# Kernel optimization log

Hardware: AMD Instinct MI355X
Metric: run time of the kernel (lower is better)

The kernel has to match this reference:

```python
import jax, jax.numpy as jnp
import numpy as np

B, D, C = 2048, 512, 50000
MARGIN = 0.3
SCALE = 30.0
EPS = 1e-12


def setup_inputs() -> dict:
    key = jax.random.key(0)
    k1, k2, k3 = jax.random.split(key, 3)
    embeddings = jax.random.normal(k1, (B, D), dtype=jnp.float32)
    labels = jax.random.randint(k2, (B,), 0, C, dtype=jnp.int64)
    # Xavier-uniform init for weight (num_classes, in_features)
    limit = float(np.sqrt(6.0 / (C + D)))
    weight = jax.random.uniform(k3, (C, D), dtype=jnp.float32, minval=-limit, maxval=limit)
    return {"embeddings": embeddings, "labels": labels, "weight": weight}


def _l2_normalize(x, axis):
    # Matches torch F.normalize(p=2, eps=1e-12): x / max(||x||, eps)
    norm = jnp.sqrt(jnp.sum(x * x, axis=axis, keepdims=True))
    return x / jnp.maximum(norm, EPS)


def reference(embeddings, labels, weight):
    emb_n = _l2_normalize(embeddings, axis=1)            # (B, D)
    w_n = _l2_normalize(weight, axis=1)                  # (C, D)
    cos = jnp.einsum("bd,cd->bc", emb_n, w_n)            # (B, C)
    # margin subtract at label index (avoid dense one-hot materialization)
    rows = jnp.arange(cos.shape[0])
    phi = cos.at[rows, labels].add(-MARGIN)
    logits = phi * SCALE
    # cross-entropy with mean reduction
    logp = jax.nn.log_softmax(logits, axis=-1)
    nll = -jnp.take_along_axis(logp, labels[:, None], axis=-1)[:, 0]
    return jnp.mean(nll)
```

## Files before the change

### kernel.cpp

```cpp
#include <hip/hip_runtime.h>
#include <hip/hip_bf16.h>
#include <math.h>
#include <stdint.h>


#define B_ROWS    2048
#define D_DIM     512
#define C_CLASSES 50000
#define C_PAD     50176
#define NCHUNK    112
#define CH_COLS   448
#define NSTRIP    14
#define ARC_MARGIN 0.3f
#define ARC_SCALE  30.0f
#define ARC_EPS    1e-12f
#define K_LOG2E_S  43.2808512f

#define OFF_WQ    0u
#define OFF_EMBQ  25690112u
#define OFF_WINV  26738688u
#define OFF_EINV  26938688u
#define OFF_PART  26946880u
#define OFF_FINP  27864384u

typedef __attribute__((ext_vector_type(8))) int   i32x8;
typedef __attribute__((ext_vector_type(4))) int   i32x4;
typedef __attribute__((ext_vector_type(4))) float f32x4;

typedef __attribute__((address_space(1))) const unsigned int g_u32;
typedef __attribute__((address_space(3))) unsigned int       l_u32;

__device__ __forceinline__ void gload_lds16(const void* g, void* l) {
    g_u32* gp = (g_u32*)(uintptr_t)g;
    l_u32* lp = (l_u32*)(uintptr_t)l;
    __builtin_amdgcn_global_load_lds(gp, lp, 16, 0, 0);
}

__global__ __launch_bounds__(256) void k_prep(const float* __restrict__ emb,
                                              const float* __restrict__ weight,
                                              uint8_t* __restrict__ embq,
                                              uint8_t* __restrict__ wq,
                                              float* __restrict__ einv,
                                              float* __restrict__ winv,
                                              float* __restrict__ out) {
    int wave = blockIdx.x * (blockDim.x >> 6) + (threadIdx.x >> 6);
    int lane = threadIdx.x & 63;
    int g0   = wave << 3;

    const float* src;
    uint8_t* dst;
    float* invout;
    if (g0 >= C_PAD) {
        int row = g0 - C_PAD;
        src = emb + (size_t)row * D_DIM;
        dst = embq + (size_t)row * D_DIM;
        invout = einv + row;
    } else if (g0 >= C_CLASSES) {
        int2 z = make_int2(0, 0);
        #pragma unroll
        for (int r = 0; r < 8; ++r)
            *(int2*)(wq + (size_t)(g0 + r) * D_DIM + lane * 8) = z;
        return;
    } else {
        src = weight + (size_t)g0 * D_DIM;
        dst = wq + (size_t)g0 * D_DIM;
        invout = winv + g0;
    }

    const float4* r4 = (const float4*)src;
    float4 v[16];
    #pragma unroll
    for (int r = 0; r < 8; ++r) {
        v[2 * r]     = r4[r * 128 + lane * 2];
        v[2 * r + 1] = r4[r * 128 + lane * 2 + 1];
    }

    #pragma unroll
    for (int r = 0; r < 8; ++r) {
        float4 v0 = v[2 * r], v1 = v[2 * r + 1];
        float s = v0.x*v0.x + v0.y*v0.y + v0.z*v0.z + v0.w*v0.w
                + v1.x*v1.x + v1.y*v1.y + v1.z*v1.z + v1.w*v1.w;
        #pragma unroll
        for (int off = 32; off; off >>= 1) s += __shfl_xor(s, off);
        float rn = 1.0f / fmaxf(sqrtf(s), ARC_EPS);
        if (lane == 0) invout[r] = rn;
        int p0 = __builtin_amdgcn_cvt_pk_fp8_f32(v0.x * rn, v0.y * rn, 0, false);
        p0     = __builtin_amdgcn_cvt_pk_fp8_f32(v0.z * rn, v0.w * rn, p0, true);
        int p1 = __builtin_amdgcn_cvt_pk_fp8_f32(v1.x * rn, v1.y * rn, 0, false);
        p1     = __builtin_amdgcn_cvt_pk_fp8_f32(v1.z * rn, v1.w * rn, p1, true);
        *(int2*)(dst + (size_t)r * D_DIM + lane * 8) = make_int2(p0, p1);
    }
}

struct TrueT  { static constexpr bool value = true;  };
struct FalseT { static constexpr bool value = false; };

__global__ __launch_bounds__(256) void k_gemm(const uint8_t* __restrict__ embq,
                                              const uint8_t* __restrict__ wq,
                                              float* __restrict__ partials) {
    __shared__ __align__(16) uint8_t Bs[2][16384];

    const int tid  = threadIdx.x;
    const int w    = tid >> 6;
    const int lane = tid & 63;
    const int c    = lane & 15;
    const int q    = lane >> 4;

    const int id  = blockIdx.x;
    const int xcd = id & 7;
    const int s   = id >> 3;
    const int ci  = s % 14;
    const int rb  = s / 14;
    const int chunk = xcd * 14 + ci;
    const int b0 = rb * 128;
    const int n0 = chunk * CH_COLS;

    const int r0 = b0 + w * 32;
    i32x8 afA[4], afB[4];
    #pragma unroll
    for (int kt = 0; kt < 4; ++kt) {
        const uint8_t* pa = embq + (size_t)(r0 + c) * D_DIM + kt * 128 + q * 32;
        const uint8_t* pb = embq + (size_t)(r0 + 16 + c) * D_DIM + kt * 128 + q * 32;
        i32x4 alo = *(const i32x4*)pa;
        i32x4 ahi = *(const i32x4*)(pa + 16);
        i32x4 blo = *(const i32x4*)pb;
        i32x4 bhi = *(const i32x4*)(pb + 16);
        afA[kt] = (i32x8){alo[0], alo[1], alo[2], alo[3], ahi[0], ahi[1], ahi[2], ahi[3]};
        afB[kt] = (i32x8){blo[0], blo[1], blo[2], blo[3], bhi[0], bhi[1], bhi[2], bhi[3]};
    }

    const int srow = c;
    const int skc  = q;
    auto stage = [&](uint8_t* dst, int st) {
        const uint8_t* base = wq + (size_t)(n0 + st * 32) * D_DIM;
        #pragma unroll
        for (int t = 0; t < 4; ++t) {
            const int p  = w * 4 + t;
            const int cb = p >> 3;
            const int h  = p & 7;
            gload_lds16(base + (size_t)(cb * 16 + srow) * D_DIM + (h * 4 + skc) * 16,
                        dst + cb * 8192 + h * 1024);
        }
    };

    f32x4 rs0 = (f32x4){0.f, 0.f, 0.f, 0.f};
    f32x4 rs1 = (f32x4){0.f, 0.f, 0.f, 0.f};

    auto compute = [&](const uint8_t* buf, int st, auto maskTag) {
        constexpr bool MASK = decltype(maskTag)::value;
        #pragma unroll
        for (int cb = 0; cb < 2; ++cb) {
            f32x4 a0 = (f32x4){0.f, 0.f, 0.f, 0.f};
            f32x4 a1 = (f32x4){0.f, 0.f, 0.f, 0.f};
            #pragma unroll
            for (int kt = 0; kt < 4; ++kt) {
                const uint8_t* p = buf + cb * 8192 + (kt * 8 + 2 * q) * 256 + c * 16;
                i32x4 lo = *(const i32x4*)p;
                i32x4 hi = *(const i32x4*)(p + 256);
                i32x8 bf = (i32x8){lo[0], lo[1], lo[2], lo[3],
                                   hi[0], hi[1], hi[2], hi[3]};
                a0 = __builtin_amdgcn_mfma_scale_f32_16x16x128_f8f6f4(
                        afA[kt], bf, a0, 0, 0, 0, 127, 0, 127);
                a1 = __builtin_amdgcn_mfma_scale_f32_16x16x128_f8f6f4(
                        afB[kt], bf, a1, 0, 0, 0, 127, 0, 127);
            }
            bool pad = false;
            if (MASK) pad = (n0 + st * 32 + cb * 16 + c) >= C_CLASSES;
            #pragma unroll
            for (int reg = 0; reg < 4; ++reg) {
                float t0 = __builtin_amdgcn_exp2f(fmaf(a0[reg], K_LOG2E_S, -K_LOG2E_S));
                float t1 = __builtin_amdgcn_exp2f(fmaf(a1[reg], K_LOG2E_S, -K_LOG2E_S));
                if (MASK && pad) { t0 = 0.f; t1 = 0.f; }
                rs0[reg] += t0;
                rs1[reg] += t1;
            }
        }
    };

    auto run = [&](auto maskTag) {
        stage(&Bs[0][0], 0);
        __syncthreads();
        #pragma unroll 1
        for (int st = 0; st < NSTRIP; st += 2) {
            stage(&Bs[1][0], st + 1);
            compute(&Bs[0][0], st, maskTag);
            __syncthreads();
            if (st + 2 < NSTRIP) stage(&Bs[0][0], st + 2);
            compute(&Bs[1][0], st + 1, maskTag);
            __syncthreads();
        }
    };
    if (chunk == NCHUNK - 1) run(TrueT{}); else run(FalseT{});

    #pragma unroll
    for (int off = 1; off < 16; off <<= 1) {
        #pragma unroll
        for (int reg = 0; reg < 4; ++reg) {
            rs0[reg] += __shfl_xor(rs0[reg], off);
            rs1[reg] += __shfl_xor(rs1[reg], off);
        }
    }
    if (c == 0) {
        #pragma unroll
        for (int reg = 0; reg < 4; ++reg) {
            partials[(size_t)(r0 + q * 4 + reg) * NCHUNK + chunk]      = rs0[reg];
            partials[(size_t)(r0 + 16 + q * 4 + reg) * NCHUNK + chunk] = rs1[reg];
        }
    }
}

__global__ __launch_bounds__(256) void k_fin(const float* __restrict__ emb,
                                             const float* __restrict__ weight,
                                             const float* __restrict__ einv,
                                             const float* __restrict__ winv,
                                             const int* __restrict__ labels,
                                             const float* __restrict__ partials,
                                             float* __restrict__ finpart) {
    __shared__ float sm[8];
    int w    = threadIdx.x >> 6;
    int lane = threadIdx.x & 63;
    int b0   = blockIdx.x * 8 + w * 2;

    int lab[2] = {labels[b0], labels[b0 + 1]};
    float4 e0[2], e1[2], w0[2], w1[2];
    float p0[2], p1[2];
    #pragma unroll
    for (int r = 0; r < 2; ++r) {
        const float4* e  = (const float4*)(emb + (size_t)(b0 + r) * D_DIM);
        const float4* wt = (const float4*)(weight + (size_t)lab[r] * D_DIM);
        e0[r] = e[lane];  e1[r] = e[lane + 64];
        w0[r] = wt[lane]; w1[r] = wt[lane + 64];
        p0[r] = partials[(size_t)(b0 + r) * NCHUNK + lane];
        p1[r] = (lane + 64 < NCHUNK)
              ? partials[(size_t)(b0 + r) * NCHUNK + lane + 64] : 0.f;
    }

    #pragma unroll
    for (int r = 0; r < 2; ++r) {
        float dot = e0[r].x*w0[r].x + e0[r].y*w0[r].y + e0[r].z*w0[r].z + e0[r].w*w0[r].w
                  + e1[r].x*w1[r].x + e1[r].y*w1[r].y + e1[r].z*w1[r].z + e1[r].w*w1[r].w;
        float ls = p0[r] + p1[r];
        #pragma unroll
        for (int off = 32; off; off >>= 1) {
            dot += __shfl_xor(dot, off);
            ls  += __shfl_xor(ls, off);
        }
        if (lane == 0) {
            int b = b0 + r;
            float cosv   = dot * einv[b] * winv[lab[r]];
            float l_orig = ARC_SCALE * cosv;
            float l_adj  = ARC_SCALE * (cosv - ARC_MARGIN);
            float s_adj = ls - __expf(l_orig - ARC_SCALE) + __expf(l_adj - ARC_SCALE);
            sm[w * 2 + r] = ARC_SCALE + logf(s_adj) - l_adj;
        }
    }
    __syncthreads();
    if (threadIdx.x == 0) {
        float t = 0.f;
        #pragma unroll
        for (int i = 0; i < 8; ++i) t += sm[i];
        finpart[blockIdx.x] = t;
    }
}

__global__ __launch_bounds__(256) void k_sum(const float* __restrict__ finpart,
                                             float* __restrict__ out) {
    __shared__ float sm[4];
    int w = threadIdx.x >> 6, lane = threadIdx.x & 63;
    float v = finpart[threadIdx.x];
    #pragma unroll
    for (int off = 32; off; off >>= 1) v += __shfl_xor(v, off);
    if (lane == 0) sm[w] = v;
    __syncthreads();
    if (threadIdx.x == 0)
        out[0] = (sm[0] + sm[1] + sm[2] + sm[3]) * (1.0f / (float)B_ROWS);
}

extern "C" void kernel_launch(void* const* d_in, const int* in_sizes, int n_in,
                              void* d_out, int out_size, void* d_ws, size_t ws_size,
                              hipStream_t stream) {
    const float* emb    = (const float*)d_in[0];
    const int*   labels = (const int*)d_in[1];
    const float* weight = (const float*)d_in[2];
    float* out = (float*)d_out;

    char* ws = (char*)d_ws;
    uint8_t* wq    = (uint8_t*)(ws + OFF_WQ);
    uint8_t* embq  = (uint8_t*)(ws + OFF_EMBQ);
    float* winv     = (float*)(ws + OFF_WINV);
    float* einv     = (float*)(ws + OFF_EINV);
    float* partials = (float*)(ws + OFF_PART);
    float* finpart  = (float*)(ws + OFF_FINP);

    k_prep<<<(C_PAD + B_ROWS) / 32, 256, 0, stream>>>(emb, weight, embq, wq,
                                                      einv, winv, out);

    k_gemm<<<1792, 256, 0, stream>>>(embq, wq, partials);

    k_fin<<<B_ROWS / 8, 256, 0, stream>>>(emb, weight, einv, winv, labels,
                                          partials, finpart);
    k_sum<<<1, 256, 0, stream>>>(finpart, out);
}
```

Baseline: 234.2 us.

## Widen GEMM strip to 64 columns with 2x2 wave layout; fuse final sum via ticket

The GEMM block now stages 64 weight columns per strip into a 32KB double buffer. Its four waves are arranged 2 rows x 2 column-halves, each wave holding 64 embedding rows (16 fp8 A fragments) and issuing 4 MFMAs per B fragment load. This doubles A-fragment reuse per LDS read, and the partial sums table doubles to 224 columns. The separate single-block sum kernel is removed: the last finishing block of k_fin, picked with an atomic ticket that k_prep resets, does the final reduction. This saves one launch but raises register pressure and LDS use, which may lower occupancy.

```diff
diff --git a/kernel.cpp b/kernel.cpp
--- a/kernel.cpp
+++ b/kernel.cpp
@@ -10,7 +10,8 @@
 #define C_PAD     50176
 #define NCHUNK    112
 #define CH_COLS   448
-#define NSTRIP    14
+#define NSTRIP    7
+#define NPART     224
 #define ARC_MARGIN 0.3f
 #define ARC_SCALE  30.0f
 #define ARC_EPS    1e-12f
@@ -21,7 +22,8 @@
 #define OFF_WINV  26738688u
 #define OFF_EINV  26938688u
 #define OFF_PART  26946880u
-#define OFF_FINP  27864384u
+#define OFF_FINP  28781888u
+#define OFF_TICK  28782912u
 
 typedef __attribute__((ext_vector_type(8))) int   i32x8;
 typedef __attribute__((ext_vector_type(4))) int   i32x4;
@@ -42,7 +44,8 @@
                                               uint8_t* __restrict__ wq,
                                               float* __restrict__ einv,
                                               float* __restrict__ winv,
-                                              float* __restrict__ out) {
+                                              unsigned int* __restrict__ ticket) {
+    if (blockIdx.x == 0 && threadIdx.x == 0) *ticket = 0u;
     int wave = blockIdx.x * (blockDim.x >> 6) + (threadIdx.x >> 6);
     int lane = threadIdx.x & 63;
     int g0   = wave << 3;
@@ -98,13 +101,15 @@
 __global__ __launch_bounds__(256) void k_gemm(const uint8_t* __restrict__ embq,
                                               const uint8_t* __restrict__ wq,
                                               float* __restrict__ partials) {
-    __shared__ __align__(16) uint8_t Bs[2][16384];
+    __shared__ __align__(16) uint8_t Bs[2][32768];
 
     const int tid  = threadIdx.x;
     const int w    = tid >> 6;
     const int lane = tid & 63;
     const int c    = lane & 15;
     const int q    = lane >> 4;
+    const int rh   = w >> 1;
+    const int ch   = w & 1;
 
     const int id  = blockIdx.x;
     const int xcd = id & 7;
@@ -115,64 +120,75 @@
     const int b0 = rb * 128;
     const int n0 = chunk * CH_COLS;
 
-    const int r0 = b0 + w * 32;
-    i32x8 afA[4], afB[4];
-    #pragma unroll
-    for (int kt = 0; kt < 4; ++kt) {
-        const uint8_t* pa = embq + (size_t)(r0 + c) * D_DIM + kt * 128 + q * 32;
-        const uint8_t* pb = embq + (size_t)(r0 + 16 + c) * D_DIM + kt * 128 + q * 32;
-        i32x4 alo = *(const i32x4*)pa;
-        i32x4 ahi = *(const i32x4*)(pa + 16);
-        i32x4 blo = *(const i32x4*)pb;
-        i32x4 bhi = *(const i32x4*)(pb + 16);
-        afA[kt] = (i32x8){alo[0], alo[1], alo[2], alo[3], ahi[0], ahi[1], ahi[2], ahi[3]};
-        afB[kt] = (i32x8){blo[0], blo[1], blo[2], blo[3], bhi[0], bhi[1], bhi[2], bhi[3]};
-    }
-
-    const int srow = c;
-    const int skc  = q;
+    const int r0 = b0 + rh * 64;
+    i32x8 af[4][4];
+    #pragma unroll
+    for (int rg = 0; rg < 4; ++rg) {
+        const uint8_t* pr = embq + (size_t)(r0 + rg * 16 + c) * D_DIM;
+        #pragma unroll
+        for (int kt = 0; kt < 4; ++kt) {
+            const uint8_t* pa = pr + kt * 128 + q * 32;
+            i32x4 lo = *(const i32x4*)pa;
+            i32x4 hi = *(const i32x4*)(pa + 16);
+            af[rg][kt] = (i32x8){lo[0], lo[1], lo[2], lo[3],
+                                 hi[0], hi[1], hi[2], hi[3]};
+        }
+    }
+
     auto stage = [&](uint8_t* dst, int st) {
-        const uint8_t* base = wq + (size_t)(n0 + st * 32) * D_DIM;
-        #pragma unroll
-        for (int t = 0; t < 4; ++t) {
-            const int p  = w * 4 + t;
-            const int cb = p >> 3;
+        const uint8_t* base = wq + (size_t)(n0 + st * 64) * D_DIM;
+        #pragma unroll
+        for (int t = 0; t < 8; ++t) {
+            const int p  = w * 8 + t;
+            const int cg = p >> 3;
             const int h  = p & 7;
-            gload_lds16(base + (size_t)(cb * 16 + srow) * D_DIM + (h * 4 + skc) * 16,
-                        dst + cb * 8192 + h * 1024);
+            gload_lds16(base + (size_t)(cg * 16 + c) * D_DIM + (h * 4 + q) * 16,
+                        dst + cg * 8192 + h * 1024);
         }
     };
 
-    f32x4 rs0 = (f32x4){0.f, 0.f, 0.f, 0.f};
-    f32x4 rs1 = (f32x4){0.f, 0.f, 0.f, 0.f};
+    f32x4 rs[4];
+    #pragma unroll
+    for (int rg = 0; rg < 4; ++rg) rs[rg] = (f32x4){0.f, 0.f, 0.f, 0.f};
 
     auto compute = [&](const uint8_t* buf, int st, auto maskTag) {
         constexpr bool MASK = decltype(maskTag)::value;
         #pragma unroll
         for (int cb = 0; cb < 2; ++cb) {
+            const int cg = ch * 2 + cb;
             f32x4 a0 = (f32x4){0.f, 0.f, 0.f, 0.f};
             f32x4 a1 = (f32x4){0.f, 0.f, 0.f, 0.f};
+            f32x4 a2 = (f32x4){0.f, 0.f, 0.f, 0.f};
+            f32x4 a3 = (f32x4){0.f, 0.f, 0.f, 0.f};
             #pragma unroll
             for (int kt = 0; kt < 4; ++kt) {
-                const uint8_t* p = buf + cb * 8192 + (kt * 8 + 2 * q) * 256 + c * 16;
+                const uint8_t* p = buf + cg * 8192 + (kt * 8 + 2 * q) * 256 + c * 16;
                 i32x4 lo = *(const i32x4*)p;
                 i32x4 hi = *(const i32x4*)(p + 256);
                 i32x8 bf = (i32x8){lo[0], lo[1], lo[2], lo[3],
                                    hi[0], hi[1], hi[2], hi[3]};
                 a0 = __builtin_amdgcn_mfma_scale_f32_16x16x128_f8f6f4(
-                        afA[kt], bf, a0, 0, 0, 0, 127, 0, 127);
+                        af[0][kt], bf, a0, 0, 0, 0, 127, 0, 127);
                 a1 = __builtin_amdgcn_mfma_scale_f32_16x16x128_f8f6f4(
-                        afB[kt], bf, a1, 0, 0, 0, 127, 0, 127);
+                        af[1][kt], bf, a1, 0, 0, 0, 127, 0, 127);
+                a2 = __builtin_amdgcn_mfma_scale_f32_16x16x128_f8f6f4(
+                        af[2][kt], bf, a2, 0, 0, 0, 127, 0, 127);
+                a3 = __builtin_amdgcn_mfma_scale_f32_16x16x128_f8f6f4(
+                        af[3][kt], bf, a3, 0, 0, 0, 127, 0, 127);
             }
             bool pad = false;
-            if (MASK) pad = (n0 + st * 32 + cb * 16 + c) >= C_CLASSES;
+            if (MASK) pad = (n0 + st * 64 + cg * 16 + c) >= C_CLASSES;
             #pragma unroll
             for (int reg = 0; reg < 4; ++reg) {
                 float t0 = __builtin_amdgcn_exp2f(fmaf(a0[reg], K_LOG2E_S, -K_LOG2E_S));
                 float t1 = __builtin_amdgcn_exp2f(fmaf(a1[reg], K_LOG2E_S, -K_LOG2E_S));
-                if (MASK && pad) { t0 = 0.f; t1 = 0.f; }
-                rs0[reg] += t0;
-                rs1[reg] += t1;
+                float t2 = __builtin_amdgcn_exp2f(fmaf(a2[reg], K_LOG2E_S, -K_LOG2E_S));
+                float t3 = __builtin_amdgcn_exp2f(fmaf(a3[reg], K_LOG2E_S, -K_LOG2E_S));
+                if (MASK && pad) { t0 = 0.f; t1 = 0.f; t2 = 0.f; t3 = 0.f; }
+                rs[0][reg] += t0;
+                rs[1][reg] += t1;
+                rs[2][reg] += t2;
+                rs[3][reg] += t3;
             }
         }
     };
@@ -182,30 +198,34 @@
         __syncthreads();
         #pragma unroll 1
         for (int st = 0; st < NSTRIP; st += 2) {
-            stage(&Bs[1][0], st + 1);
+            if (st + 1 < NSTRIP) stage(&Bs[1][0], st + 1);
             compute(&Bs[0][0], st, maskTag);
             __syncthreads();
             if (st + 2 < NSTRIP) stage(&Bs[0][0], st + 2);
-            compute(&Bs[1][0], st + 1, maskTag);
-            __syncthreads();
+            if (st + 1 < NSTRIP) {
+                compute(&Bs[1][0], st + 1, maskTag);
+                __syncthreads();
+            }
         }
     };
     if (chunk == NCHUNK - 1) run(TrueT{}); else run(FalseT{});
 
     #pragma unroll
-    for (int off = 1; off < 16; off <<= 1) {
-        #pragma unroll
-        for (int reg = 0; reg < 4; ++reg) {
-            rs0[reg] += __shfl_xor(rs0[reg], off);
-            rs1[reg] += __shfl_xor(rs1[reg], off);
-        }
-    }
+    for (int off = 1; off < 16; off <<= 1)
+        #pragma unroll
+        for (int rg = 0; rg < 4; ++rg)
+            #pragma unroll
+            for (int reg = 0; reg < 4; ++reg)
+                rs[rg][reg] += __shfl_xor(rs[rg][reg], off);
+
     if (c == 0) {
-        #pragma unroll
-        for (int reg = 0; reg < 4; ++reg) {
-            partials[(size_t)(r0 + q * 4 + reg) * NCHUNK + chunk]      = rs0[reg];
-            partials[(size_t)(r0 + 16 + q * 4 + reg) * NCHUNK + chunk] = rs1[reg];
-        }
+        const int pcol = chunk * 2 + ch;
+        #pragma unroll
+        for (int rg = 0; rg < 4; ++rg)
+            #pragma unroll
+            for (int reg = 0; reg < 4; ++reg)
+                partials[(size_t)(r0 + rg * 16 + q * 4 + reg) * NPART + pcol]
+                    = rs[rg][reg];
     }
 }
 
@@ -215,31 +235,37 @@
                                              const float* __restrict__ winv,
                                              const int* __restrict__ labels,
                                              const float* __restrict__ partials,
-                                             float* __restrict__ finpart) {
+                                             float* __restrict__ finpart,
+                                             unsigned int* __restrict__ ticket,
+                                             float* __restrict__ out) {
     __shared__ float sm[8];
+    __shared__ int is_last;
     int w    = threadIdx.x >> 6;
     int lane = threadIdx.x & 63;
     int b0   = blockIdx.x * 8 + w * 2;
 
     int lab[2] = {labels[b0], labels[b0 + 1]};
     float4 e0[2], e1[2], w0[2], w1[2];
-    float p0[2], p1[2];
+    float p[2][4];
     #pragma unroll
     for (int r = 0; r < 2; ++r) {
         const float4* e  = (const float4*)(emb + (size_t)(b0 + r) * D_DIM);
         const float4* wt = (const float4*)(weight + (size_t)lab[r] * D_DIM);
         e0[r] = e[lane];  e1[r] = e[lane + 64];
         w0[r] = wt[lane]; w1[r] = wt[lane + 64];
-        p0[r] = partials[(size_t)(b0 + r) * NCHUNK + lane];
-        p1[r] = (lane + 64 < NCHUNK)
-              ? partials[(size_t)(b0 + r) * NCHUNK + lane + 64] : 0.f;
+        #pragma unroll
+        for (int t = 0; t < 4; ++t) {
+            int idx = lane + t * 64;
+            p[r][t] = (idx < NPART)
+                    ? partials[(size_t)(b0 + r) * NPART + idx] : 0.f;
+        }
     }
 
     #pragma unroll
     for (int r = 0; r < 2; ++r) {
         float dot = e0[r].x*w0[r].x + e0[r].y*w0[r].y + e0[r].z*w0[r].z + e0[r].w*w0[r].w
                   + e1[r].x*w1[r].x + e1[r].y*w1[r].y + e1[r].z*w1[r].z + e1[r].w*w1[r].w;
-        float ls = p0[r] + p1[r];
+        float ls = p[r][0] + p[r][1] + p[r][2] + p[r][3];
         #pragma unroll
         for (int off = 32; off; off >>= 1) {
             dot += __shfl_xor(dot, off);
@@ -260,20 +286,22 @@
         #pragma unroll
         for (int i = 0; i < 8; ++i) t += sm[i];
         finpart[blockIdx.x] = t;
-    }
-}
-
-__global__ __launch_bounds__(256) void k_sum(const float* __restrict__ finpart,
-                                             float* __restrict__ out) {
-    __shared__ float sm[4];
-    int w = threadIdx.x >> 6, lane = threadIdx.x & 63;
-    float v = finpart[threadIdx.x];
-    #pragma unroll
-    for (int off = 32; off; off >>= 1) v += __shfl_xor(v, off);
-    if (lane == 0) sm[w] = v;
+        __threadfence();
+        unsigned int old = atomicAdd(ticket, 1u);
+        is_last = (old == gridDim.x - 1) ? 1 : 0;
+    }
     __syncthreads();
-    if (threadIdx.x == 0)
-        out[0] = (sm[0] + sm[1] + sm[2] + sm[3]) * (1.0f / (float)B_ROWS);
+    if (is_last) {
+        __threadfence();
+        volatile const float* fp = finpart;
+        float v = fp[threadIdx.x];
+        #pragma unroll
+        for (int off = 32; off; off >>= 1) v += __shfl_xor(v, off);
+        if (lane == 0) sm[w] = v;
+        __syncthreads();
+        if (threadIdx.x == 0)
+            out[0] = (sm[0] + sm[1] + sm[2] + sm[3]) * (1.0f / (float)B_ROWS);
+    }
 }
 
 extern "C" void kernel_launch(void* const* d_in, const int* in_sizes, int n_in,
@@ -291,13 +319,13 @@
     float* einv     = (float*)(ws + OFF_EINV);
     float* partials = (float*)(ws + OFF_PART);
     float* finpart  = (float*)(ws + OFF_FINP);
+    unsigned int* ticket = (unsigned int*)(ws + OFF_TICK);
 
     k_prep<<<(C_PAD + B_ROWS) / 32, 256, 0, stream>>>(emb, weight, embq, wq,
-                                                      einv, winv, out);
+                                                      einv, winv, ticket);
 
     k_gemm<<<1792, 256, 0, stream>>>(embq, wq, partials);
 
     k_fin<<<B_ROWS / 8, 256, 0, stream>>>(emb, weight, einv, winv, labels,
-                                          partials, finpart);
-    k_sum<<<1, 256, 0, stream>>>(finpart, out);
-}
+                                          partials, finpart, ticket, out);
+}
```

Result: slower. 276.7 us (+18.2%).

## Triple-buffer GEMM LDS staging and fold final sum into fin kernel

Applied to the files above, without the earlier changes.

The GEMM's weight-tile staging moves from a double buffer with two block barriers per strip pair to a three-slot ring. Each strip now uses a single barrier with an explicit vmcnt wait, so loads run two strips ahead of compute. Separately, the single-block k_sum launch is dropped: k_fin blocks take an atomic ticket and the last block performs the final reduction, saving one kernel launch. This raises LDS use to 48KB per block, which may lower occupancy, and relies on a ticket that k_prep resets.

```diff
diff --git a/kernel.cpp b/kernel.cpp
--- a/kernel.cpp
+++ b/kernel.cpp
@@ -22,6 +22,7 @@
 #define OFF_EINV  26938688u
 #define OFF_PART  26946880u
 #define OFF_FINP  27864384u
+#define OFF_TICK  27865408u
 
 typedef __attribute__((ext_vector_type(8))) int   i32x8;
 typedef __attribute__((ext_vector_type(4))) int   i32x4;
@@ -42,7 +43,8 @@
                                               uint8_t* __restrict__ wq,
                                               float* __restrict__ einv,
                                               float* __restrict__ winv,
-                                              float* __restrict__ out) {
+                                              unsigned int* __restrict__ ticket) {
+    if (blockIdx.x == 0 && threadIdx.x == 0) *ticket = 0u;
     int wave = blockIdx.x * (blockDim.x >> 6) + (threadIdx.x >> 6);
     int lane = threadIdx.x & 63;
     int g0   = wave << 3;
@@ -98,7 +100,7 @@
 __global__ __launch_bounds__(256) void k_gemm(const uint8_t* __restrict__ embq,
                                               const uint8_t* __restrict__ wq,
                                               float* __restrict__ partials) {
-    __shared__ __align__(16) uint8_t Bs[2][16384];
+    __shared__ __align__(16) uint8_t Bs[3][16384];
 
     const int tid  = threadIdx.x;
     const int w    = tid >> 6;
@@ -129,16 +131,14 @@
         afB[kt] = (i32x8){blo[0], blo[1], blo[2], blo[3], bhi[0], bhi[1], bhi[2], bhi[3]};
     }
 
-    const int srow = c;
-    const int skc  = q;
     auto stage = [&](uint8_t* dst, int st) {
-        const uint8_t* base = wq + (size_t)(n0 + st * 32) * D_DIM;
+        const uint8_t* base_ = wq + (size_t)(n0 + st * 32) * D_DIM;
         #pragma unroll
         for (int t = 0; t < 4; ++t) {
             const int p  = w * 4 + t;
             const int cb = p >> 3;
             const int h  = p & 7;
-            gload_lds16(base + (size_t)(cb * 16 + srow) * D_DIM + (h * 4 + skc) * 16,
+            gload_lds16(base_ + (size_t)(cb * 16 + c) * D_DIM + (h * 4 + q) * 16,
                         dst + cb * 8192 + h * 1024);
         }
     };
@@ -178,17 +178,24 @@
     };
 
     auto run = [&](auto maskTag) {
-        stage(&Bs[0][0], 0);
-        __syncthreads();
+        uint8_t* p0 = &Bs[0][0];
+        uint8_t* p1 = &Bs[1][0];
+        uint8_t* p2 = &Bs[2][0];
+        stage(p0, 0);
+        stage(p1, 1);
         #pragma unroll 1
-        for (int st = 0; st < NSTRIP; st += 2) {
-            stage(&Bs[1][0], st + 1);
-            compute(&Bs[0][0], st, maskTag);
-            __syncthreads();
-            if (st + 2 < NSTRIP) stage(&Bs[0][0], st + 2);
-            compute(&Bs[1][0], st + 1, maskTag);
-            __syncthreads();
-        }
+        for (int st = 0; st < NSTRIP - 1; ++st) {
+            asm volatile("s_waitcnt vmcnt(4)" ::: "memory");
+            __builtin_amdgcn_s_barrier();
+            __builtin_amdgcn_sched_barrier(0);
+            if (st + 2 < NSTRIP) stage(p2, st + 2);
+            compute(p0, st, maskTag);
+            uint8_t* t = p0; p0 = p1; p1 = p2; p2 = t;
+        }
+        asm volatile("s_waitcnt vmcnt(0)" ::: "memory");
+        __builtin_amdgcn_s_barrier();
+        __builtin_amdgcn_sched_barrier(0);
+        compute(p0, NSTRIP - 1, maskTag);
     };
     if (chunk == NCHUNK - 1) run(TrueT{}); else run(FalseT{});
 
@@ -215,8 +222,11 @@
                                              const float* __restrict__ winv,
                                              const int* __restrict__ labels,
                                              const float* __restrict__ partials,
-                                             float* __restrict__ finpart) {
+                                             float* __restrict__ finpart,
+                                             unsigned int* __restrict__ ticket,
+                                             float* __restrict__ out) {
     __shared__ float sm[8];
+    __shared__ int is_last;
     int w    = threadIdx.x >> 6;
     int lane = threadIdx.x & 63;
     int b0   = blockIdx.x * 8 + w * 2;
@@ -260,20 +270,22 @@
         #pragma unroll
         for (int i = 0; i < 8; ++i) t += sm[i];
         finpart[blockIdx.x] = t;
-    }
-}
-
-__global__ __launch_bounds__(256) void k_sum(const float* __restrict__ finpart,
-                                             float* __restrict__ out) {
-    __shared__ float sm[4];
-    int w = threadIdx.x >> 6, lane = threadIdx.x & 63;
-    float v = finpart[threadIdx.x];
-    #pragma unroll
-    for (int off = 32; off; off >>= 1) v += __shfl_xor(v, off);
-    if (lane == 0) sm[w] = v;
+        __threadfence();
+        unsigned int old = atomicAdd(ticket, 1u);
+        is_last = (old == gridDim.x - 1) ? 1 : 0;
+    }
     __syncthreads();
-    if (threadIdx.x == 0)
-        out[0] = (sm[0] + sm[1] + sm[2] + sm[3]) * (1.0f / (float)B_ROWS);
+    if (is_last) {
+        __threadfence();
+        volatile const float* fp = finpart;
+        float v = fp[threadIdx.x];
+        #pragma unroll
+        for (int off = 32; off; off >>= 1) v += __shfl_xor(v, off);
+        if (lane == 0) sm[w] = v;
+        __syncthreads();
+        if (threadIdx.x == 0)
+            out[0] = (sm[0] + sm[1] + sm[2] + sm[3]) * (1.0f / (float)B_ROWS);
+    }
 }
 
 extern "C" void kernel_launch(void* const* d_in, const int* in_sizes, int n_in,
@@ -291,13 +303,13 @@
     float* einv     = (float*)(ws + OFF_EINV);
     float* partials = (float*)(ws + OFF_PART);
     float* finpart  = (float*)(ws + OFF_FINP);
+    unsigned int* ticket = (unsigned int*)(ws + OFF_TICK);
 
     k_prep<<<(C_PAD + B_ROWS) / 32, 256, 0, stream>>>(emb, weight, embq, wq,
-                                                      einv, winv, out);
+                                                      einv, winv, ticket);
 
     k_gemm<<<1792, 256, 0, stream>>>(embq, wq, partials);
 
     k_fin<<<B_ROWS / 8, 256, 0, stream>>>(emb, weight, einv, winv, labels,
-                                          partials, finpart);
-    k_sum<<<1, 256, 0, stream>>>(finpart, out);
-}
+                                          partials, finpart, ticket, out);
+}
```

Result: no change. 233.7 us (-0.2%).
